# Performance work log

Hardware: AMD Instinct MI355X
Metric: run time of the kernel (lower is better)

Reference implementation:

```python
import jax, jax.numpy as jnp
import numpy as np

N_GRID = 512
B = 4
NUM_VIEWS = 4
EPS = 1e-6


def _build_mesh(n):
    # grid mesh with |v| in (0, 0.9] so log(|v|/(1-|v|)) is finite and sign(v) != 0
    xs = np.linspace(-0.9, 0.9, n, dtype=np.float32)  # 512 points -> no exact zero
    X, Y = np.meshgrid(xs, xs, indexing='ij')
    Z = 0.1 * np.abs(np.sin(3.0 * X) * np.cos(3.0 * Y)) + 0.01
    V = np.stack([X, Y, Z], -1).reshape(-1, 3).astype(np.float32)
    idx = np.arange(n * n).reshape(n, n)
    v00, v01 = idx[:-1, :-1].ravel(), idx[:-1, 1:].ravel()
    v10, v11 = idx[1:, :-1].ravel(), idx[1:, 1:].ravel()
    f1 = np.stack([v00, v10, v01], -1)
    f2 = np.stack([v10, v11, v01], -1)
    F = np.concatenate([f1, f2], 0).astype(np.int64)
    return V, F


def _topology(F, nv):
    # per-face edges + the opposite vertex of each edge within its face
    e = np.concatenate([F[:, [0, 1]], F[:, [1, 2]], F[:, [2, 0]]], 0)
    opp = np.concatenate([F[:, 2], F[:, 0], F[:, 1]], 0)
    key = np.sort(e, axis=1)
    uniq, inv, counts = np.unique(key, axis=0, return_inverse=True, return_counts=True)
    # LaplacianLoss: unique neighbor pairs (matrix assignment dedups), both directions
    src = np.concatenate([uniq[:, 0], uniq[:, 1]]).astype(np.int32)
    dst = np.concatenate([uniq[:, 1], uniq[:, 0]]).astype(np.int32)
    deg = np.bincount(dst, minlength=nv).astype(np.int32)
    # FlattenLoss: edges shared by exactly two faces -> (v0,v1) edge, (v2,v3) opposite verts
    order = np.argsort(inv, kind='stable')
    starts = np.searchsorted(inv[order], np.arange(len(uniq)))
    m2 = counts == 2
    i1 = order[starts[m2]]
    i2 = order[starts[m2] + 1]
    v0s = uniq[m2, 0].astype(np.int32)
    v1s = uniq[m2, 1].astype(np.int32)
    v2s = opp[i1].astype(np.int32)
    v3s = opp[i2].astype(np.int32)
    return src, dst, deg, v0s, v1s, v2s, v3s


def setup_inputs() -> dict:
    key = jax.random.key(0)
    k1, k2, k3 = jax.random.split(key, 3)
    Vt, F = _build_mesh(N_GRID)
    nv = Vt.shape[0]
    src, dst, deg, v0s, v1s, v2s, v3s = _topology(F, nv)
    return {
        'displace': jax.random.normal(k1, (B, nv, 3), jnp.float32) * 0.1,
        'center': jax.random.normal(k2, (B, 1, 3), jnp.float32) * 0.1,
        'texture': jax.random.uniform(k3, (B, nv, 3), jnp.float32),
        'template_vertices': jnp.asarray(Vt)[None],  # [1, V, 3]
        'lap_src': jnp.asarray(src),
        'lap_dst': jnp.asarray(dst),
        'deg': jnp.asarray(deg),
        'v0s': jnp.asarray(v0s),
        'v1s': jnp.asarray(v1s),
        'v2s': jnp.asarray(v2s),
        'v3s': jnp.asarray(v3s),
        'num_views': NUM_VIEWS,
    }


def reference(displace, center, texture, template_vertices, lap_src, lap_dst, deg,
              v0s, v1s, v2s, v3s, num_views):
    nv = template_vertices.shape[1]
    tv = template_vertices  # [1, V, 3]
    # vertex warp (elementwise)
    base = jnp.log(jnp.abs(tv) / (1.0 - jnp.abs(tv)))
    centroid = jnp.tanh(center)  # [B, 1, 3]
    v = jax.nn.sigmoid(base + displace) * jnp.sign(tv)  # [B, V, 3]
    v = jax.nn.relu(v) * (1.0 - centroid) - jax.nn.relu(-v) * (centroid + 1.0)
    v = v + centroid

    # uniform Laplacian loss: Lx = x - mean(neighbors); sum of squares per batch, mean over batch
    inv_deg = 1.0 / deg.astype(v.dtype)

    def lap_one(x):  # x: [V, 3]
        nbr = jax.ops.segment_sum(x[lap_src], lap_dst, num_segments=nv)
        return x - nbr * inv_deg[:, None]

    lx = jax.vmap(lap_one)(v)
    lap_loss = jnp.mean(jnp.sum(lx * lx, axis=(1, 2)))

    # flatten loss over face pairs sharing an edge
    p0, p1, p2, p3 = v[:, v0s], v[:, v1s], v[:, v2s], v[:, v3s]  # [B, P, 3]
    a1 = p1 - p0
    a1l2 = jnp.sum(a1 * a1, -1)
    a1l1 = jnp.sqrt(a1l2 + EPS)

    def _comp(b):
        bl2 = jnp.sum(b * b, -1)
        bl1 = jnp.sqrt(bl2 + EPS)
        ab = jnp.sum(a1 * b, -1)
        cos = ab / (a1l1 * bl1 + EPS)
        sin = jnp.sqrt(1.0 - cos * cos + EPS)
        cb = b - a1 * (ab / (a1l2 + EPS))[..., None]
        return cb, bl1 * sin

    cb1, l1 = _comp(p2 - p0)
    cb2, l2 = _comp(p3 - p0)
    cos = jnp.sum(cb1 * cb2, -1) / (l1 * l2 + EPS)
    flat_loss = jnp.mean(jnp.sum((cos + 1.0) ** 2, axis=1))

    # torch repeat(1, numViews, 1).reshape(numViews*B, V, 3) == tile then reshape
    b = v.shape[0]
    verts_out = jnp.tile(v, (1, num_views, 1)).reshape(num_views * b, nv, 3)
    tex_out = jnp.tile(texture, (1, num_views, 1)).reshape(num_views * b, nv, 3)
    return verts_out, tex_out, lap_loss, flat_loss
```

## Files before the change

kernel.cpp:

```cpp
#include <hip/hip_runtime.h>

#define NGRID 512
#define NV (NGRID * NGRID)
#define NB 4
#define NVIEWS 4
#define FEPS 1e-6f
#define TR 8
#define LDS_ROWS (TR + 2)
#define ROWF (NGRID * 3)
#define LDSF (LDS_ROWS * ROWF)

static constexpr size_t NVF3 = (size_t)NV * 3;
static constexpr size_t VERTS_FLOATS = (size_t)NVIEWS * NB * NVF3;
static constexpr size_t LAP_OFF = 2 * VERTS_FLOATS;
static constexpr size_t FLAT_OFF = LAP_OFF + 1;

__global__ void init_losses(float* __restrict__ out) {
    if (threadIdx.x == 0) {
        out[LAP_OFF] = 0.0f;
        out[FLAT_OFF] = 0.0f;
    }
}

__device__ __forceinline__ float3 ldsP(const float* __restrict__ vs, int lr, int c) {
    const int o = lr * ROWF + c * 3;
    return make_float3(vs[o], vs[o + 1], vs[o + 2]);
}

__device__ __forceinline__ float edge_val(float3 p0, float3 p1, float3 p2, float3 p3) {
    const float a1x = p1.x - p0.x, a1y = p1.y - p0.y, a1z = p1.z - p0.z;
    const float a1l2 = a1x * a1x + a1y * a1y + a1z * a1z;
    const float a1l1 = sqrtf(a1l2 + FEPS);
    const float inv_a1l2 = 1.0f / (a1l2 + FEPS);

    const float b1x = p2.x - p0.x, b1y = p2.y - p0.y, b1z = p2.z - p0.z;
    const float b1l2 = b1x * b1x + b1y * b1y + b1z * b1z;
    const float b1l1 = sqrtf(b1l2 + FEPS);
    const float ab1 = a1x * b1x + a1y * b1y + a1z * b1z;
    const float cos1 = ab1 / (a1l1 * b1l1 + FEPS);
    const float sin1 = sqrtf(1.0f - cos1 * cos1 + FEPS);
    const float f1 = ab1 * inv_a1l2;
    const float cb1x = b1x - a1x * f1, cb1y = b1y - a1y * f1, cb1z = b1z - a1z * f1;
    const float l1 = b1l1 * sin1;

    const float b2x = p3.x - p0.x, b2y = p3.y - p0.y, b2z = p3.z - p0.z;
    const float b2l2 = b2x * b2x + b2y * b2y + b2z * b2z;
    const float b2l1 = sqrtf(b2l2 + FEPS);
    const float ab2 = a1x * b2x + a1y * b2y + a1z * b2z;
    const float cos2 = ab2 / (a1l1 * b2l1 + FEPS);
    const float sin2 = sqrtf(1.0f - cos2 * cos2 + FEPS);
    const float f2 = ab2 * inv_a1l2;
    const float cb2x = b2x - a1x * f2, cb2y = b2y - a1y * f2, cb2z = b2z - a1z * f2;
    const float l2 = b2l1 * sin2;

    const float cosd = (cb1x * cb2x + cb1y * cb2y + cb1z * cb2z) / (l1 * l2 + FEPS);
    const float t = cosd + 1.0f;
    return t * t;
}

__global__ __launch_bounds__(256, 2) void mesh_fused_kernel(
    const float* __restrict__ disp, const float* __restrict__ center,
    const float* __restrict__ tex, const float* __restrict__ tv,
    float* __restrict__ out)
{
    __shared__ float vs[LDSF];
    const int tid = threadIdx.x;
    const int b = blockIdx.y;
    const int R0 = blockIdx.x * TR;

    const float c0 = tanhf(center[b * 3 + 0]);
    const float c1 = tanhf(center[b * 3 + 1]);
    const float c2 = tanhf(center[b * 3 + 2]);
    const float carr[3] = {c0, c1, c2};

    {
        const float4* __restrict__ tv4 = (const float4*)tv;
        const float4* __restrict__ d4p = (const float4*)(disp + (size_t)b * NVF3);
        float4* __restrict__ vs4 = (float4*)vs;
        const int start4 = (R0 - 1) * (ROWF / 4);
        for (int ff4 = tid; ff4 < LDSF / 4; ff4 += 256) {
            const int g4 = start4 + ff4;
            if (g4 < 0 || g4 >= (int)(NVF3 / 4)) continue;
            const float4 t = tv4[g4];
            const float4 d = d4p[g4];
            const float tvv[4] = {t.x, t.y, t.z, t.w};
            const float dvv[4] = {d.x, d.y, d.z, d.w};
            float vr[4];
            int comp = ff4 % 3;
#pragma unroll
            for (int l = 0; l < 4; ++l) {
                const float tvl = tvv[l];
                const float s = fabsf(tvl);
                const float sgn = (tvl > 0.0f) ? 1.0f : -1.0f;
                const float v0 = sgn * (s / (s + (1.0f - s) * expf(-dvv[l])));
                const float c = carr[comp];
                const float pos = fmaxf(v0, 0.0f);
                const float neg = fmaxf(-v0, 0.0f);
                vr[l] = pos * (1.0f - c) - neg * (c + 1.0f) + c;
                comp = (comp == 2) ? 0 : comp + 1;
            }
            vs4[ff4] = make_float4(vr[0], vr[1], vr[2], vr[3]);
        }
    }
    __syncthreads();

    {
        const float4* __restrict__ vs4 = (const float4*)vs;
        const float4* __restrict__ t4p = (const float4*)(tex + (size_t)b * NVF3);
        float4* __restrict__ out4 = (float4*)out;
        const size_t blk4 = NVF3 / 4;
        const int tile_base4 = R0 * (ROWF / 4);
#pragma unroll 1
        for (int q = tid; q < TR * ROWF / 4; q += 256) {
            const float4 vo = vs4[ROWF / 4 + q];
            const float4 tx = t4p[tile_base4 + q];
            const size_t pos4 = (size_t)tile_base4 + q;
#pragma unroll
            for (int view = 0; view < NVIEWS; ++view) {
                const size_t base = (size_t)(b * NVIEWS + view) * blk4;
                out4[base + pos4] = vo;
                out4[(VERTS_FLOATS / 4) + base + pos4] = tx;
            }
        }
    }

    float lap_sum = 0.0f, flat_sum = 0.0f;
    for (int it = 0; it < TR * NGRID / 256; ++it) {
        const int idx = it * 256 + tid;
        const int r_off = idx >> 9;
        const int c = idx & (NGRID - 1);
        const int gr = R0 + r_off;
        const int lr = r_off + 1;

        const float3 pc = ldsP(vs, lr, c);

        {
            float sx = 0.f, sy = 0.f, sz = 0.f;
            int deg = 0;
            if (gr > 0)               { float3 p = ldsP(vs, lr - 1, c);     sx += p.x; sy += p.y; sz += p.z; deg++; }
            if (gr < NGRID - 1)       { float3 p = ldsP(vs, lr + 1, c);     sx += p.x; sy += p.y; sz += p.z; deg++; }
            if (c > 0)                { float3 p = ldsP(vs, lr, c - 1);     sx += p.x; sy += p.y; sz += p.z; deg++; }
            if (c < NGRID - 1)        { float3 p = ldsP(vs, lr, c + 1);     sx += p.x; sy += p.y; sz += p.z; deg++; }
            if (gr > 0 && c < NGRID - 1)      { float3 p = ldsP(vs, lr - 1, c + 1); sx += p.x; sy += p.y; sz += p.z; deg++; }
            if (gr < NGRID - 1 && c > 0)      { float3 p = ldsP(vs, lr + 1, c - 1); sx += p.x; sy += p.y; sz += p.z; deg++; }
            const float id = 1.0f / (float)deg;
            const float lx = pc.x - sx * id;
            const float ly = pc.y - sy * id;
            const float lz = pc.z - sz * id;
            lap_sum += lx * lx + ly * ly + lz * lz;
        }

        if (gr < NGRID - 1 && c < NGRID - 1) {
            flat_sum += edge_val(ldsP(vs, lr, c + 1), ldsP(vs, lr + 1, c),
                                 pc,                  ldsP(vs, lr + 1, c + 1));
        }
        if (gr >= 1 && gr < NGRID - 1 && c < NGRID - 1) {
            flat_sum += edge_val(pc, ldsP(vs, lr, c + 1),
                                 ldsP(vs, lr + 1, c), ldsP(vs, lr - 1, c + 1));
        }
        if (gr < NGRID - 1 && c >= 1 && c < NGRID - 1) {
            flat_sum += edge_val(pc, ldsP(vs, lr + 1, c),
                                 ldsP(vs, lr, c + 1), ldsP(vs, lr + 1, c - 1));
        }
    }

#pragma unroll
    for (int off = 32; off > 0; off >>= 1) {
        lap_sum  += __shfl_down(lap_sum, off, 64);
        flat_sum += __shfl_down(flat_sum, off, 64);
    }
    __shared__ float red[8];
    const int lane = tid & 63;
    const int wid = tid >> 6;
    if (lane == 0) { red[wid] = lap_sum; red[4 + wid] = flat_sum; }
    __syncthreads();
    if (tid == 0) {
        const float ls = red[0] + red[1] + red[2] + red[3];
        const float fs = red[4] + red[5] + red[6] + red[7];
        atomicAdd(&out[LAP_OFF],  ls * (1.0f / NB));
        atomicAdd(&out[FLAT_OFF], fs * (1.0f / NB));
    }
}

extern "C" void kernel_launch(void* const* d_in, const int* in_sizes, int n_in,
                              void* d_out, int out_size, void* d_ws, size_t ws_size,
                              hipStream_t stream)
{
    const float* disp   = (const float*)d_in[0];
    const float* center = (const float*)d_in[1];
    const float* tex    = (const float*)d_in[2];
    const float* tv     = (const float*)d_in[3];
    float* out = (float*)d_out;

    init_losses<<<1, 64, 0, stream>>>(out);
    mesh_fused_kernel<<<dim3(NGRID / TR, NB), 256, 0, stream>>>(disp, center, tex, tv, out);
}
```

Before: 200.3 us.

## Shrink row tile to 2, use nontemporal loads/stores, fully unroll staging loops

Cuts the rows per block from 8 to 2, which gives four times as many blocks for better occupancy and latency hiding. The price is more halo recomputation, since 4 rows are staged for every 2 output rows. Texture reads and the replicated vertex and texture writes now use nontemporal builtins so the large streaming output is kept out of the caches. The fixed-trip staging and copy loops are fully unrolled, and the launch bounds drop the min-blocks hint.

```diff
diff --git a/kernel.cpp b/kernel.cpp
--- a/kernel.cpp
+++ b/kernel.cpp
@@ -5,10 +5,12 @@
 #define NB 4
 #define NVIEWS 4
 #define FEPS 1e-6f
-#define TR 8
+#define TR 2
 #define LDS_ROWS (TR + 2)
 #define ROWF (NGRID * 3)
 #define LDSF (LDS_ROWS * ROWF)
+
+typedef float fvec4 __attribute__((ext_vector_type(4)));
 
 static constexpr size_t NVF3 = (size_t)NV * 3;
 static constexpr size_t VERTS_FLOATS = (size_t)NVIEWS * NB * NVF3;
@@ -58,7 +60,7 @@
     return t * t;
 }
 
-__global__ __launch_bounds__(256, 2) void mesh_fused_kernel(
+__global__ __launch_bounds__(256) void mesh_fused_kernel(
     const float* __restrict__ disp, const float* __restrict__ center,
     const float* __restrict__ tex, const float* __restrict__ tv,
     float* __restrict__ out)
@@ -74,57 +76,59 @@
     const float carr[3] = {c0, c1, c2};
 
     {
-        const float4* __restrict__ tv4 = (const float4*)tv;
-        const float4* __restrict__ d4p = (const float4*)(disp + (size_t)b * NVF3);
-        float4* __restrict__ vs4 = (float4*)vs;
+        const fvec4* __restrict__ tv4 = (const fvec4*)tv;
+        const fvec4* __restrict__ d4p = (const fvec4*)(disp + (size_t)b * NVF3);
+        fvec4* __restrict__ vs4 = (fvec4*)vs;
         const int start4 = (R0 - 1) * (ROWF / 4);
-        for (int ff4 = tid; ff4 < LDSF / 4; ff4 += 256) {
+#pragma unroll
+        for (int ss = 0; ss < LDSF / 4 / 256; ++ss) {
+            const int ff4 = ss * 256 + tid;
             const int g4 = start4 + ff4;
             if (g4 < 0 || g4 >= (int)(NVF3 / 4)) continue;
-            const float4 t = tv4[g4];
-            const float4 d = d4p[g4];
-            const float tvv[4] = {t.x, t.y, t.z, t.w};
-            const float dvv[4] = {d.x, d.y, d.z, d.w};
-            float vr[4];
+            const fvec4 t = tv4[g4];
+            const fvec4 d = d4p[g4];
+            fvec4 vr;
             int comp = ff4 % 3;
 #pragma unroll
             for (int l = 0; l < 4; ++l) {
-                const float tvl = tvv[l];
+                const float tvl = t[l];
                 const float s = fabsf(tvl);
                 const float sgn = (tvl > 0.0f) ? 1.0f : -1.0f;
-                const float v0 = sgn * (s / (s + (1.0f - s) * expf(-dvv[l])));
+                const float v0 = sgn * (s / (s + (1.0f - s) * expf(-d[l])));
                 const float c = carr[comp];
                 const float pos = fmaxf(v0, 0.0f);
                 const float neg = fmaxf(-v0, 0.0f);
                 vr[l] = pos * (1.0f - c) - neg * (c + 1.0f) + c;
                 comp = (comp == 2) ? 0 : comp + 1;
             }
-            vs4[ff4] = make_float4(vr[0], vr[1], vr[2], vr[3]);
+            vs4[ff4] = vr;
         }
     }
     __syncthreads();
 
     {
-        const float4* __restrict__ vs4 = (const float4*)vs;
-        const float4* __restrict__ t4p = (const float4*)(tex + (size_t)b * NVF3);
-        float4* __restrict__ out4 = (float4*)out;
+        const fvec4* __restrict__ vs4 = (const fvec4*)vs;
+        const fvec4* __restrict__ t4p = (const fvec4*)(tex + (size_t)b * NVF3);
+        fvec4* __restrict__ out4 = (fvec4*)out;
         const size_t blk4 = NVF3 / 4;
         const int tile_base4 = R0 * (ROWF / 4);
-#pragma unroll 1
-        for (int q = tid; q < TR * ROWF / 4; q += 256) {
-            const float4 vo = vs4[ROWF / 4 + q];
-            const float4 tx = t4p[tile_base4 + q];
+#pragma unroll
+        for (int qq = 0; qq < TR * ROWF / 4 / 256; ++qq) {
+            const int q = qq * 256 + tid;
+            const fvec4 vo = vs4[ROWF / 4 + q];
+            const fvec4 tx = __builtin_nontemporal_load(&t4p[tile_base4 + q]);
             const size_t pos4 = (size_t)tile_base4 + q;
 #pragma unroll
             for (int view = 0; view < NVIEWS; ++view) {
                 const size_t base = (size_t)(b * NVIEWS + view) * blk4;
-                out4[base + pos4] = vo;
-                out4[(VERTS_FLOATS / 4) + base + pos4] = tx;
+                __builtin_nontemporal_store(vo, &out4[base + pos4]);
+                __builtin_nontemporal_store(tx, &out4[(VERTS_FLOATS / 4) + base + pos4]);
             }
         }
     }
 
     float lap_sum = 0.0f, flat_sum = 0.0f;
+#pragma unroll 1
     for (int it = 0; it < TR * NGRID / 256; ++it) {
         const int idx = it * 256 + tid;
         const int r_off = idx >> 9;
```

New measurement: 184.2 us. 1.09x faster.
